# Kernel tuning notes

Hardware: AMD Instinct MI355X
Metric: run time of the kernel (lower is better)

## Reference

```python
import jax, jax.numpy as jnp
import numpy as np

N = 50000        # nodes
E = 800000       # edges (avg degree 16)
IN = 128         # n_feat
C0, H0 = 32, 4   # layer0: out_channels, heads (concat -> 128)
C1, H1 = 32, 1   # layer1: out_channels, heads (mean)
NEG_SLOPE = 0.2


def setup_inputs() -> dict:
    key = jax.random.key(0)
    ks = jax.random.split(key, 16)
    def p(k, shape, fan):
        return jax.random.normal(k, shape, jnp.float32) / np.float32(np.sqrt(fan))
    x = jax.random.normal(ks[0], (N, IN), jnp.float32)
    edge_index = jax.random.randint(ks[1], (2, E), 0, N, dtype=jnp.int32)
    return {
        "x": x,
        "edge_index": edge_index,
        # layer 0 GATConv: in=128 -> 4 heads x 32, concat
        "W0": p(ks[2], (H0 * C0, IN), IN),
        "att_src0": p(ks[3], (H0, C0), C0),
        "att_dst0": p(ks[4], (H0, C0), C0),
        "bias0": jnp.zeros((H0 * C0,), jnp.float32),
        "linW0": p(ks[5], (H0 * C0, IN), IN),
        "linb0": jnp.zeros((H0 * C0,), jnp.float32),
        # layer 1 GATConv: in=128 -> 1 head x 32, mean
        "W1": p(ks[6], (H1 * C1, H0 * C0), H0 * C0),
        "att_src1": p(ks[7], (H1, C1), C1),
        "att_dst1": p(ks[8], (H1, C1), C1),
        "bias1": jnp.zeros((C1,), jnp.float32),
        "linW1": p(ks[9], (C1, H0 * C0), H0 * C0),
        "linb1": jnp.zeros((C1,), jnp.float32),
    }


def gat_conv(x, src, dst, W, att_src, att_dst, bias, concat):
    """PyG-style GATConv (self-loops already appended to src/dst)."""
    n = x.shape[0]
    H, C = att_src.shape
    h = (x @ W.T).reshape(n, H, C)                       # [N,H,C]
    a_src = jnp.einsum('nhc,hc->nh', h, att_src)          # [N,H]
    a_dst = jnp.einsum('nhc,hc->nh', h, att_dst)          # [N,H]
    e = jax.nn.leaky_relu(a_src[src] + a_dst[dst], NEG_SLOPE)  # [E,H]
    # segment softmax over incoming edges of each dst node
    m = jax.ops.segment_max(e, dst, num_segments=n)       # [N,H]
    ex = jnp.exp(e - m[dst])
    denom = jax.ops.segment_sum(ex, dst, num_segments=n)  # [N,H]
    alpha = ex / (denom[dst] + 1e-16)                     # [E,H]
    out = jax.ops.segment_sum(h[src] * alpha[:, :, None], dst, num_segments=n)  # [N,H,C]
    out = out.reshape(n, H * C) if concat else out.mean(axis=1)
    return out + bias


def reference(x, edge_index, W0, att_src0, att_dst0, bias0, linW0, linb0,
              W1, att_src1, att_dst1, bias1, linW1, linb1):
    n = x.shape[0]
    loop = jnp.arange(n, dtype=edge_index.dtype)
    src = jnp.concatenate([edge_index[0], loop])  # add self-loops
    dst = jnp.concatenate([edge_index[1], loop])
    # layer 0: conv + linear skip, then ELU (eval mode -> dropout is a no-op)
    h = gat_conv(x, src, dst, W0, att_src0, att_dst0, bias0, True) + x @ linW0.T + linb0
    h = jax.nn.elu(h)
    # layer 1 (last): conv + linear skip, no activation
    out = gat_conv(h, src, dst, W1, att_src1, att_dst1, bias1, False) + h @ linW1.T + linb1
    return out
```

## Files before the change

kernel.cpp:

```cpp
#include <hip/hip_runtime.h>
#include <hip/hip_bf16.h>


typedef __attribute__((ext_vector_type(8))) short bf8_t;
typedef __attribute__((ext_vector_type(4))) float f4_t;
typedef __attribute__((ext_vector_type(2))) float f2_t;

#define NBUCK 256
#define BCAP  8192
#define TSTR  136

__device__ inline short f2bf(float f) {
    return (short)__builtin_bit_cast(unsigned short, __float2bfloat16(f));
}
__device__ inline float blo(unsigned int p) { return __uint_as_float(p << 16); }
__device__ inline float bhi(unsigned int p) { return __uint_as_float(p & 0xffff0000u); }
__device__ inline float lrexp(float e) {
    e = (e > 0.f) ? e : 0.2f * e;
    return __expf(e);
}

__global__ __launch_bounds__(256) void k_pack(
    const float* __restrict__ W0, const float* __restrict__ lW0,
    const float* __restrict__ W1, const float* __restrict__ lW1,
    const float* __restrict__ b0, const float* __restrict__ lb0,
    const float* __restrict__ b1, const float* __restrict__ lb1,
    short* __restrict__ Wp0, short* __restrict__ lWp0,
    short* __restrict__ Wp1, short* __restrict__ lWp1,
    float* __restrict__ bc0, float* __restrict__ bc1,
    int* __restrict__ gcur) {
    int tid = threadIdx.x;
    int i = blockIdx.x * 256 + tid;
    {
        int j = i & 7, lane = (i >> 3) & 63, kc = i >> 9;
        int kb = kc & 3, ct = kc >> 2;
        int src = (ct * 16 + (lane & 15)) * 128 + kb * 32 + (lane >> 4) * 8 + j;
        Wp0[i]  = f2bf(W0[src]);
        lWp0[i] = f2bf(lW0[src]);
        if (i < 4096) {
            Wp1[i]  = f2bf(W1[src]);
            lWp1[i] = f2bf(lW1[src]);
        }
    }
    if (blockIdx.x == 0) gcur[tid] = 0;
    if (i < 128) bc0[i] = b0[i] + lb0[i];
    else if (i < 160) bc1[i - 128] = b1[i - 128] + lb1[i - 128];
}

__global__ __launch_bounds__(256) void k_bg(
    const int* __restrict__ ei,
    const float* __restrict__ x,
    const short* __restrict__ Wp0, const short* __restrict__ lWp0,
    const float* __restrict__ as0, const float* __restrict__ ad0,
    int* __restrict__ gcur, unsigned int* __restrict__ bucketed,
    unsigned char* __restrict__ h0f8, __hip_bfloat16* __restrict__ skipb,
    float* __restrict__ a0s, float* __restrict__ a0d,
    int E, int T, int NBBK, int N) {
    __shared__ int hist[NBUCK];
    __shared__ int gbase[NBUCK];
    __shared__ short tile[4][16 * TSTR];
    __shared__ unsigned char t8[4][16 * 136];
    int tid = threadIdx.x;

    if ((int)blockIdx.x < NBBK) {
        int bb = blockIdx.x;
        hist[tid] = 0;
        __syncthreads();
        int base = bb * 2048;
        unsigned int pk[8]; int rk[8]; int bk[8];
        #pragma unroll
        for (int j = 0; j < 8; j++) {
            int e = base + j * 256 + tid;
            if (e < T) {
                int src, dst;
                if (e < E) { src = ei[e]; dst = ei[E + e]; }
                else       { src = e - E; dst = src; }
                int b = dst >> 8;
                pk[j] = ((unsigned int)dst << 16) | (unsigned int)src;
                bk[j] = b;
                rk[j] = atomicAdd(&hist[b], 1);
            } else bk[j] = -1;
        }
        __syncthreads();
        int h = hist[tid];
        if (h > 0) gbase[tid] = tid * BCAP + atomicAdd(&gcur[tid], h);
        __syncthreads();
        #pragma unroll
        for (int j = 0; j < 8; j++)
            if (bk[j] >= 0)
                bucketed[gbase[bk[j]] + rk[j]] = pk[j];
        return;
    }

    int bx = blockIdx.x - NBBK;
    int wv = tid >> 6, lane = tid & 63;
    int rowbase = bx * 64 + wv * 16;
    int m = lane & 15, q = lane >> 4;
    int arow = rowbase + m; if (arow >= N) arow = N - 1;
    bf8_t a[4];
    #pragma unroll
    for (int kb = 0; kb < 4; kb++) {
        const float4* px = (const float4*)(x + (size_t)arow * 128 + kb * 32 + q * 8);
        float4 lo = px[0], hi = px[1];
        bf8_t f;
        f[0] = f2bf(lo.x); f[1] = f2bf(lo.y); f[2] = f2bf(lo.z); f[3] = f2bf(lo.w);
        f[4] = f2bf(hi.x); f[5] = f2bf(hi.y); f[6] = f2bf(hi.z); f[7] = f2bf(hi.w);
        a[kb] = f;
    }
    float sacc[4][4], dacc[4][4];
    #pragma unroll
    for (int h = 0; h < 4; h++)
        #pragma unroll
        for (int r = 0; r < 4; r++) { sacc[h][r] = 0.f; dacc[h][r] = 0.f; }
    short* tl = tile[wv];
    unsigned char* t8l = t8[wv];
    int r4 = lane >> 2, qt = lane & 3;
    int drow = rowbase + r4;

    #pragma unroll
    for (int ct = 0; ct < 8; ct++) {
        f4_t acc = {0.f, 0.f, 0.f, 0.f};
        #pragma unroll
        for (int kb = 0; kb < 4; kb++) {
            bf8_t b = *(const bf8_t*)(Wp0 + (((ct * 4 + kb) * 64 + lane) << 3));
            acc = __builtin_amdgcn_mfma_f32_16x16x32_bf16(a[kb], b, acc, 0, 0, 0);
        }
        int hd = ct >> 1;
        float ws = as0[ct * 16 + m], wd = ad0[ct * 16 + m];
        #pragma unroll
        for (int r = 0; r < 4; r++) {
            sacc[hd][r] += acc[r] * ws;
            dacc[hd][r] += acc[r] * wd;
            int pk8 = __builtin_amdgcn_cvt_pk_fp8_f32(acc[r], acc[r], 0, false);
            t8l[(q * 4 + r) * 136 + ct * 16 + m] = (unsigned char)(pk8 & 0xff);
        }
    }
    if (drow < N) {
        const unsigned char* sp8 = t8l + r4 * 136 + qt * 32;
        uint2 w0 = ((const uint2*)sp8)[0];
        uint2 w1 = ((const uint2*)sp8)[1];
        uint2 w2 = ((const uint2*)sp8)[2];
        uint2 w3 = ((const uint2*)sp8)[3];
        uint4 o0 = make_uint4(w0.x, w0.y, w1.x, w1.y);
        uint4 o1 = make_uint4(w2.x, w2.y, w3.x, w3.y);
        unsigned char* dst = h0f8 + (size_t)drow * 128 + qt * 32;
        *(uint4*)dst = o0;
        *(uint4*)(dst + 16) = o1;
    }

    #pragma unroll
    for (int ct = 0; ct < 8; ct++) {
        f4_t acc = {0.f, 0.f, 0.f, 0.f};
        #pragma unroll
        for (int kb = 0; kb < 4; kb++) {
            bf8_t b = *(const bf8_t*)(lWp0 + (((ct * 4 + kb) * 64 + lane) << 3));
            acc = __builtin_amdgcn_mfma_f32_16x16x32_bf16(a[kb], b, acc, 0, 0, 0);
        }
        #pragma unroll
        for (int r = 0; r < 4; r++)
            tl[(q * 4 + r) * TSTR + ct * 16 + m] = f2bf(acc[r]);
    }
    if (drow < N) {
        short* dst = (short*)skipb + (size_t)drow * 128 + qt * 32;
        const short* srcp = tl + r4 * TSTR + qt * 32;
        #pragma unroll
        for (int s = 0; s < 4; s++)
            *(uint4*)(dst + s * 8) = *(const uint4*)(srcp + s * 8);
    }

    #pragma unroll
    for (int h = 0; h < 4; h++)
        #pragma unroll
        for (int r = 0; r < 4; r++) {
            float s = sacc[h][r], d = dacc[h][r];
            #pragma unroll
            for (int off = 1; off < 16; off <<= 1) {
                s += __shfl_xor(s, off);
                d += __shfl_xor(d, off);
            }
            sacc[h][r] = s; dacc[h][r] = d;
        }
    if (m < 4) {
        #pragma unroll
        for (int r = 0; r < 4; r++) {
            int row = rowbase + q * 4 + r;
            if (row < N) {
                float sv = (m == 0) ? sacc[0][r] : (m == 1) ? sacc[1][r]
                         : (m == 2) ? sacc[2][r] : sacc[3][r];
                float dv = (m == 0) ? dacc[0][r] : (m == 1) ? dacc[1][r]
                         : (m == 2) ? dacc[2][r] : dacc[3][r];
                a0s[row * 4 + m] = sv;
                a0d[row * 4 + m] = dv;
            }
        }
    }
}

__global__ __launch_bounds__(256) void k_fill(
    const unsigned int* __restrict__ bucketed, const int* __restrict__ gcur,
    int* __restrict__ rowstart, unsigned short* __restrict__ esrc, int N) {
    __shared__ int ihist[256];
    __shared__ int incl[256];
    int b = blockIdx.x, t = threadIdx.x;
    int nodebase = b << 8;
    int cntt = gcur[t];
    incl[t] = cntt;
    __syncthreads();
    for (int off = 1; off < 256; off <<= 1) {
        int tv = (t >= off) ? incl[t - off] : 0;
        __syncthreads();
        incl[t] += tv;
        __syncthreads();
    }
    int rbase = (b > 0) ? incl[b - 1] : 0;
    if (b == 0 && t == 255) rowstart[N] = incl[255];
    int used = gcur[b];
    const unsigned int* bk = bucketed + (size_t)b * BCAP;
    __syncthreads();
    ihist[t] = 0;
    __syncthreads();
    for (int i = t; i < used; i += 256)
        atomicAdd(&ihist[(bk[i] >> 16) - nodebase], 1);
    __syncthreads();
    int v = ihist[t];
    incl[t] = v;
    __syncthreads();
    for (int off = 1; off < 256; off <<= 1) {
        int tv = (t >= off) ? incl[t - off] : 0;
        __syncthreads();
        incl[t] += tv;
        __syncthreads();
    }
    int myexcl = incl[t] - v;
    int node = nodebase + t;
    if (node < N) rowstart[node] = rbase + myexcl;
    __syncthreads();
    ihist[t] = myexcl;
    __syncthreads();
    for (int i = t; i < used; i += 256) {
        unsigned int p = bk[i];
        int pos = atomicAdd(&ihist[(p >> 16) - nodebase], 1);
        esrc[rbase + pos] = (unsigned short)(p & 0xffffu);
    }
}

__global__ __launch_bounds__(256) void k_aggfuse(
    const int* __restrict__ rowstart, const unsigned short* __restrict__ esrc,
    const uint2* __restrict__ h0f8,
    const float* __restrict__ a0s, const float* __restrict__ a0d,
    const float* __restrict__ bc0,
    const unsigned int* __restrict__ skip0,
    const short* __restrict__ Wp1, const short* __restrict__ lWp1,
    const float* __restrict__ as1, const float* __restrict__ ad1,
    __hip_bfloat16* __restrict__ h1, float* __restrict__ outskip,
    float* __restrict__ a1s, float* __restrict__ a1d, int n) {
    __shared__ __align__(16) short hrow[16][136];
    __shared__ __align__(16) short th[16 * 40];
    __shared__ __align__(16) float ts[16 * 36];
    __shared__ float satt[2][16], datt[2][16];

    int tid = threadIdx.x;
    int nl = tid >> 4, t = tid & 15, hd = t >> 2;
    int rowbase = blockIdx.x << 4;
    int node = rowbase + nl;

    if (node < n) {
        float ad = a0d[node * 4 + hd];
        int s0 = rowstart[node], s1 = rowstart[node + 1];
        float den = 0.f;
        float acc[8];
        #pragma unroll
        for (int k = 0; k < 8; k++) acc[k] = 0.f;
        int i = s0;
        for (; i + 3 < s1; i += 4) {
            int sE[4]; float e[4]; uint2 p[4];
            #pragma unroll
            for (int j = 0; j < 4; j++) sE[j] = esrc[i + j];
            #pragma unroll
            for (int j = 0; j < 4; j++) e[j] = a0s[sE[j] * 4 + hd] + ad;
            #pragma unroll
            for (int j = 0; j < 4; j++) p[j] = h0f8[(size_t)sE[j] * 16 + t];
            #pragma unroll
            for (int j = 0; j < 4; j++) {
                float wgt = lrexp(e[j]);
                den += wgt;
                f2_t c01 = __builtin_amdgcn_cvt_pk_f32_fp8(p[j].x, false);
                f2_t c23 = __builtin_amdgcn_cvt_pk_f32_fp8(p[j].x, true);
                f2_t c45 = __builtin_amdgcn_cvt_pk_f32_fp8(p[j].y, false);
                f2_t c67 = __builtin_amdgcn_cvt_pk_f32_fp8(p[j].y, true);
                acc[0] += wgt * c01.x; acc[1] += wgt * c01.y;
                acc[2] += wgt * c23.x; acc[3] += wgt * c23.y;
                acc[4] += wgt * c45.x; acc[5] += wgt * c45.y;
                acc[6] += wgt * c67.x; acc[7] += wgt * c67.y;
            }
        }
        for (; i < s1; ++i) {
            int s = esrc[i];
            float wgt = lrexp(a0s[s * 4 + hd] + ad);
            uint2 p = h0f8[(size_t)s * 16 + t];
            den += wgt;
            f2_t c01 = __builtin_amdgcn_cvt_pk_f32_fp8(p.x, false);
            f2_t c23 = __builtin_amdgcn_cvt_pk_f32_fp8(p.x, true);
            f2_t c45 = __builtin_amdgcn_cvt_pk_f32_fp8(p.y, false);
            f2_t c67 = __builtin_amdgcn_cvt_pk_f32_fp8(p.y, true);
            acc[0] += wgt * c01.x; acc[1] += wgt * c01.y;
            acc[2] += wgt * c23.x; acc[3] += wgt * c23.y;
            acc[4] += wgt * c45.x; acc[5] += wgt * c45.y;
            acc[6] += wgt * c67.x; acc[7] += wgt * c67.y;
        }
        float inv = 1.0f / (den + 1e-16f);
        uint4 sp = *(const uint4*)(skip0 + (size_t)node * 64 + t * 4);
        int c0 = t * 8;
        float o[8];
        o[0] = acc[0] * inv + blo(sp.x) + bc0[c0 + 0];
        o[1] = acc[1] * inv + bhi(sp.x) + bc0[c0 + 1];
        o[2] = acc[2] * inv + blo(sp.y) + bc0[c0 + 2];
        o[3] = acc[3] * inv + bhi(sp.y) + bc0[c0 + 3];
        o[4] = acc[4] * inv + blo(sp.z) + bc0[c0 + 4];
        o[5] = acc[5] * inv + bhi(sp.z) + bc0[c0 + 5];
        o[6] = acc[6] * inv + blo(sp.w) + bc0[c0 + 6];
        o[7] = acc[7] * inv + bhi(sp.w) + bc0[c0 + 7];
        #pragma unroll
        for (int k = 0; k < 8; k++)
            o[k] = (o[k] > 0.f) ? o[k] : (__expf(o[k]) - 1.f);
        uint4 res;
        res.x = (unsigned int)(unsigned short)f2bf(o[0]) | ((unsigned int)(unsigned short)f2bf(o[1]) << 16);
        res.y = (unsigned int)(unsigned short)f2bf(o[2]) | ((unsigned int)(unsigned short)f2bf(o[3]) << 16);
        res.z = (unsigned int)(unsigned short)f2bf(o[4]) | ((unsigned int)(unsigned short)f2bf(o[5]) << 16);
        res.w = (unsigned int)(unsigned short)f2bf(o[6]) | ((unsigned int)(unsigned short)f2bf(o[7]) << 16);
        *(uint4*)&hrow[nl][t * 8] = res;
    } else {
        *(uint4*)&hrow[nl][t * 8] = make_uint4(0u, 0u, 0u, 0u);
    }
    __syncthreads();

    int wv = tid >> 6, lane = tid & 63;
    int m = lane & 15, q = lane >> 4;
    bf8_t a[4];
    #pragma unroll
    for (int kb = 0; kb < 4; kb++)
        a[kb] = *(const bf8_t*)&hrow[m][kb * 32 + q * 8];
    int ct = wv & 1;
    const short* Wt = (wv < 2) ? Wp1 : lWp1;
    f4_t acc = {0.f, 0.f, 0.f, 0.f};
    #pragma unroll
    for (int kb = 0; kb < 4; kb++) {
        bf8_t b = *(const bf8_t*)(Wt + (((ct * 4 + kb) * 64 + lane) << 3));
        acc = __builtin_amdgcn_mfma_f32_16x16x32_bf16(a[kb], b, acc, 0, 0, 0);
    }
    if (wv < 2) {
        float wsv = as1[ct * 16 + m], wdv = ad1[ct * 16 + m];
        #pragma unroll
        for (int r = 0; r < 4; r++) {
            th[(q * 4 + r) * 40 + ct * 16 + m] = f2bf(acc[r]);
            float s = acc[r] * wsv, d = acc[r] * wdv;
            #pragma unroll
            for (int off = 1; off < 16; off <<= 1) {
                s += __shfl_xor(s, off);
                d += __shfl_xor(d, off);
            }
            if (m == 0) { satt[ct][q * 4 + r] = s; datt[ct][q * 4 + r] = d; }
        }
    } else {
        #pragma unroll
        for (int r = 0; r < 4; r++)
            ts[(q * 4 + r) * 36 + ct * 16 + m] = acc[r];
    }
    __syncthreads();

    if (tid < 64) {
        int row = tid >> 2, qt = tid & 3;
        if (rowbase + row < n)
            *(uint4*)((short*)h1 + (size_t)(rowbase + row) * 32 + qt * 8) =
                *(const uint4*)&th[row * 40 + qt * 8];
    } else if (tid < 192) {
        int i2 = tid - 64, row = i2 >> 3, qt = i2 & 7;
        if (rowbase + row < n)
            *(uint4*)(outskip + (size_t)(rowbase + row) * 32 + qt * 4) =
                *(const uint4*)&ts[row * 36 + qt * 4];
    } else if (tid < 208) {
        int r2 = tid - 192;
        if (rowbase + r2 < n) {
            a1s[rowbase + r2] = satt[0][r2] + satt[1][r2];
            a1d[rowbase + r2] = datt[0][r2] + datt[1][r2];
        }
    }
}

__global__ __launch_bounds__(256) void k_agg1(
    const int* __restrict__ rowstart, const unsigned short* __restrict__ esrc,
    const __hip_bfloat16* __restrict__ h1,
    const float* __restrict__ a1s, const float* __restrict__ a1d,
    const float* __restrict__ bc1,
    float* __restrict__ out, int n) {
    int node = (blockIdx.x * 256 + threadIdx.x) >> 6;
    int lane = threadIdx.x & 63;
    if (node >= n) return;
    int g = lane >> 4, t = lane & 15;
    float ad = a1d[node];
    int s0 = rowstart[node], s1 = rowstart[node + 1];
    const unsigned int* h1w = (const unsigned int*)h1;
    float den = 0.f, acc0 = 0.f, acc1 = 0.f;
    int i = s0 + g;
    for (; i + 12 < s1; i += 16) {
        int sE[4]; float e[4]; unsigned int p[4];
        #pragma unroll
        for (int j = 0; j < 4; j++) sE[j] = esrc[i + 4 * j];
        #pragma unroll
        for (int j = 0; j < 4; j++) e[j] = a1s[sE[j]] + ad;
        #pragma unroll
        for (int j = 0; j < 4; j++) p[j] = h1w[(size_t)sE[j] * 16 + t];
        #pragma unroll
        for (int j = 0; j < 4; j++) {
            float wgt = lrexp(e[j]);
            den += wgt;
            acc0 += wgt * blo(p[j]);
            acc1 += wgt * bhi(p[j]);
        }
    }
    for (; i < s1; i += 4) {
        int s = esrc[i];
        float wv = lrexp(a1s[s] + ad);
        unsigned int p = h1w[(size_t)s * 16 + t];
        den += wv; acc0 += wv * blo(p); acc1 += wv * bhi(p);
    }
    acc0 += __shfl_xor(acc0, 16); acc0 += __shfl_xor(acc0, 32);
    acc1 += __shfl_xor(acc1, 16); acc1 += __shfl_xor(acc1, 32);
    den  += __shfl_xor(den, 16);  den  += __shfl_xor(den, 32);
    if (g == 0) {
        float inv = 1.0f / (den + 1e-16f);
        int c0 = t * 2;
        size_t idx = (size_t)node * 32 + c0;
        float2 sk = *(const float2*)(out + idx);
        float2 r;
        r.x = acc0 * inv + sk.x + bc1[c0];
        r.y = acc1 * inv + sk.y + bc1[c0 + 1];
        *(float2*)(out + idx) = r;
    }
}


extern "C" void kernel_launch(void* const* d_in, const int* in_sizes, int n_in,
                              void* d_out, int out_size, void* d_ws, size_t ws_size,
                              hipStream_t stream) {
    const float* x   = (const float*)d_in[0];
    const int*   ei  = (const int*)d_in[1];
    const float* W0  = (const float*)d_in[2];
    const float* as0 = (const float*)d_in[3];
    const float* ad0 = (const float*)d_in[4];
    const float* b0  = (const float*)d_in[5];
    const float* lW0 = (const float*)d_in[6];
    const float* lb0 = (const float*)d_in[7];
    const float* W1  = (const float*)d_in[8];
    const float* as1 = (const float*)d_in[9];
    const float* ad1 = (const float*)d_in[10];
    const float* b1  = (const float*)d_in[11];
    const float* lW1 = (const float*)d_in[12];
    const float* lb1 = (const float*)d_in[13];
    float* out = (float*)d_out;

    const int N = in_sizes[0] / 128;
    const int E = in_sizes[1] / 2;
    const int T = E + N;
    const int NBK  = (N + 255) >> 8;
    const int NBBK = (T + 2047) / 2048;
    const int NG0  = (N + 63) / 64;

    char* w = (char*)d_ws;
    auto alloc = [&](size_t bytes) -> char* {
        char* p = w; w += (bytes + 255) / 256 * 256; return p;
    };
    int* rowstart  = (int*)alloc((size_t)(N + 1) * 4);
    int* gcur      = (int*)alloc(NBUCK * 4);
    unsigned int* bucketed = (unsigned int*)alloc((size_t)NBUCK * BCAP * 4);
    unsigned short* esrc = (unsigned short*)alloc((size_t)T * 2);
    float* aS      = (float*)alloc((size_t)N * 4 * 4);
    float* aD      = (float*)alloc((size_t)N * 4 * 4);
    char* hbuf     = alloc((size_t)N * 128);
    __hip_bfloat16* skip0 = (__hip_bfloat16*)alloc((size_t)N * 128 * 2);
    __hip_bfloat16* h1buf = (__hip_bfloat16*)alloc((size_t)N * 32 * 2);
    float* aS1     = (float*)alloc((size_t)N * 4);
    float* aD1     = (float*)alloc((size_t)N * 4);
    short* Wp0  = (short*)alloc(16384 * 2);
    short* lWp0 = (short*)alloc(16384 * 2);
    short* Wp1  = (short*)alloc(4096 * 2);
    short* lWp1 = (short*)alloc(4096 * 2);
    float* bc0  = (float*)alloc(128 * 4);
    float* bc1  = (float*)alloc(32 * 4);

    k_pack<<<64, 256, 0, stream>>>(W0, lW0, W1, lW1, b0, lb0, b1, lb1,
                                   Wp0, lWp0, Wp1, lWp1, bc0, bc1, gcur);
    k_bg<<<NBBK + NG0, 256, 0, stream>>>(
        ei, x, Wp0, lWp0, as0, ad0, gcur, bucketed,
        (unsigned char*)hbuf, skip0, aS, aD, E, T, NBBK, N);
    k_fill<<<NBK, 256, 0, stream>>>(bucketed, gcur, rowstart, esrc, N);
    k_aggfuse<<<(N + 15) / 16, 256, 0, stream>>>(
        rowstart, esrc, (const uint2*)hbuf, aS, aD, bc0,
        (const unsigned int*)skip0, Wp1, lWp1, as1, ad1,
        h1buf, out, aS1, aD1, N);
    k_agg1<<<(N + 3) / 4, 256, 0, stream>>>(rowstart, esrc, h1buf,
                                            aS1, aD1, bc1, out, N);
}
```

Measured before the change: 198.0 us.

## Split layer-0 GEMM across bucketing and fill kernels to overlap stages

Moves the layer-0 GEMM body into a shared device function and splits its rows. The first GSPLIT rows still run in the bucketing kernel, and the rest run as extra blocks in the CSR fill kernel. This lets the small, sync-heavy fill kernel (196 blocks) share the GPU with GEMM work so the machine stays busier. LDS is merged into one aliased buffer, which needs an added __syncthreads between the fp8 and bf16 tile phases. The hardcoded split point assumes N is above GSPLIT and tunes the load balance to this input size.

```diff
diff --git a/kernel.cpp b/kernel.cpp
--- a/kernel.cpp
+++ b/kernel.cpp
@@ -9,6 +9,7 @@
 #define NBUCK 256
 #define BCAP  8192
 #define TSTR  136
+#define GSPLIT 29952
 
 __device__ inline short f2bf(float f) {
     return (short)__builtin_bit_cast(unsigned short, __float2bfloat16(f));
@@ -47,6 +48,118 @@
     else if (i < 160) bc1[i - 128] = b1[i - 128] + lb1[i - 128];
 }
 
+__device__ __forceinline__ void gemm0_block(
+    int rowbase0, int tid, char* lds,
+    const float* __restrict__ x,
+    const short* __restrict__ Wp0, const short* __restrict__ lWp0,
+    const float* __restrict__ as0, const float* __restrict__ ad0,
+    unsigned char* __restrict__ h0f8, __hip_bfloat16* __restrict__ skipb,
+    float* __restrict__ a0s, float* __restrict__ a0d, int N) {
+    int wv = tid >> 6, lane = tid & 63;
+    int rowbase = rowbase0 + wv * 16;
+    int m = lane & 15, q = lane >> 4;
+    int arow = rowbase + m; if (arow >= N) arow = N - 1;
+    bf8_t a[4];
+    #pragma unroll
+    for (int kb = 0; kb < 4; kb++) {
+        const float4* px = (const float4*)(x + (size_t)arow * 128 + kb * 32 + q * 8);
+        float4 lo = px[0], hi = px[1];
+        bf8_t f;
+        f[0] = f2bf(lo.x); f[1] = f2bf(lo.y); f[2] = f2bf(lo.z); f[3] = f2bf(lo.w);
+        f[4] = f2bf(hi.x); f[5] = f2bf(hi.y); f[6] = f2bf(hi.z); f[7] = f2bf(hi.w);
+        a[kb] = f;
+    }
+    float sacc[4][4], dacc[4][4];
+    #pragma unroll
+    for (int h = 0; h < 4; h++)
+        #pragma unroll
+        for (int r = 0; r < 4; r++) { sacc[h][r] = 0.f; dacc[h][r] = 0.f; }
+    char* wslice = lds + wv * 4352;
+    short* tl = (short*)wslice;
+    unsigned char* t8l = (unsigned char*)wslice;
+    int r4 = lane >> 2, qt = lane & 3;
+    int drow = rowbase + r4;
+
+    #pragma unroll
+    for (int ct = 0; ct < 8; ct++) {
+        f4_t acc = {0.f, 0.f, 0.f, 0.f};
+        #pragma unroll
+        for (int kb = 0; kb < 4; kb++) {
+            bf8_t b = *(const bf8_t*)(Wp0 + (((ct * 4 + kb) * 64 + lane) << 3));
+            acc = __builtin_amdgcn_mfma_f32_16x16x32_bf16(a[kb], b, acc, 0, 0, 0);
+        }
+        int hd = ct >> 1;
+        float ws = as0[ct * 16 + m], wd = ad0[ct * 16 + m];
+        #pragma unroll
+        for (int r = 0; r < 4; r++) {
+            sacc[hd][r] += acc[r] * ws;
+            dacc[hd][r] += acc[r] * wd;
+            int pk8 = __builtin_amdgcn_cvt_pk_fp8_f32(acc[r], acc[r], 0, false);
+            t8l[(q * 4 + r) * 136 + ct * 16 + m] = (unsigned char)(pk8 & 0xff);
+        }
+    }
+    if (drow < N) {
+        const unsigned char* sp8 = t8l + r4 * 136 + qt * 32;
+        uint2 w0 = ((const uint2*)sp8)[0];
+        uint2 w1 = ((const uint2*)sp8)[1];
+        uint2 w2 = ((const uint2*)sp8)[2];
+        uint2 w3 = ((const uint2*)sp8)[3];
+        uint4 o0 = make_uint4(w0.x, w0.y, w1.x, w1.y);
+        uint4 o1 = make_uint4(w2.x, w2.y, w3.x, w3.y);
+        unsigned char* dst = h0f8 + (size_t)drow * 128 + qt * 32;
+        *(uint4*)dst = o0;
+        *(uint4*)(dst + 16) = o1;
+    }
+    __syncthreads();
+
+    #pragma unroll
+    for (int ct = 0; ct < 8; ct++) {
+        f4_t acc = {0.f, 0.f, 0.f, 0.f};
+        #pragma unroll
+        for (int kb = 0; kb < 4; kb++) {
+            bf8_t b = *(const bf8_t*)(lWp0 + (((ct * 4 + kb) * 64 + lane) << 3));
+            acc = __builtin_amdgcn_mfma_f32_16x16x32_bf16(a[kb], b, acc, 0, 0, 0);
+        }
+        #pragma unroll
+        for (int r = 0; r < 4; r++)
+            tl[(q * 4 + r) * TSTR + ct * 16 + m] = f2bf(acc[r]);
+    }
+    if (drow < N) {
+        short* dst = (short*)skipb + (size_t)drow * 128 + qt * 32;
+        const short* srcp = tl + r4 * TSTR + qt * 32;
+        #pragma unroll
+        for (int s = 0; s < 4; s++)
+            *(uint4*)(dst + s * 8) = *(const uint4*)(srcp + s * 8);
+    }
+
+    #pragma unroll
+    for (int h = 0; h < 4; h++)
+        #pragma unroll
+        for (int r = 0; r < 4; r++) {
+            float s = sacc[h][r], d = dacc[h][r];
+            #pragma unroll
+            for (int off = 1; off < 16; off <<= 1) {
+                s += __shfl_xor(s, off);
+                d += __shfl_xor(d, off);
+            }
+            sacc[h][r] = s; dacc[h][r] = d;
+        }
+    if (m < 4) {
+        #pragma unroll
+        for (int r = 0; r < 4; r++) {
+            int row = rowbase + q * 4 + r;
+            if (row < N) {
+                float sv = (m == 0) ? sacc[0][r] : (m == 1) ? sacc[1][r]
+                         : (m == 2) ? sacc[2][r] : sacc[3][r];
+                float dv = (m == 0) ? dacc[0][r] : (m == 1) ? dacc[1][r]
+                         : (m == 2) ? dacc[2][r] : dacc[3][r];
+                a0s[row * 4 + m] = sv;
+                a0d[row * 4 + m] = dv;
+            }
+        }
+    }
+}
+
 __global__ __launch_bounds__(256) void k_bg(
     const int* __restrict__ ei,
     const float* __restrict__ x,
@@ -56,13 +169,12 @@
     unsigned char* __restrict__ h0f8, __hip_bfloat16* __restrict__ skipb,
     float* __restrict__ a0s, float* __restrict__ a0d,
     int E, int T, int NBBK, int N) {
-    __shared__ int hist[NBUCK];
-    __shared__ int gbase[NBUCK];
-    __shared__ short tile[4][16 * TSTR];
-    __shared__ unsigned char t8[4][16 * 136];
+    __shared__ __align__(16) char lds[17408];
     int tid = threadIdx.x;
 
     if ((int)blockIdx.x < NBBK) {
+        int* hist  = (int*)lds;
+        int* gbase = (int*)(lds + 1024);
         int bb = blockIdx.x;
         hist[tid] = 0;
         __syncthreads();
@@ -92,156 +204,73 @@
         return;
     }
 
-    int bx = blockIdx.x - NBBK;
-    int wv = tid >> 6, lane = tid & 63;
-    int rowbase = bx * 64 + wv * 16;
-    int m = lane & 15, q = lane >> 4;
-    int arow = rowbase + m; if (arow >= N) arow = N - 1;
-    bf8_t a[4];
-    #pragma unroll
-    for (int kb = 0; kb < 4; kb++) {
-        const float4* px = (const float4*)(x + (size_t)arow * 128 + kb * 32 + q * 8);
-        float4 lo = px[0], hi = px[1];
-        bf8_t f;
-        f[0] = f2bf(lo.x); f[1] = f2bf(lo.y); f[2] = f2bf(lo.z); f[3] = f2bf(lo.w);
-        f[4] = f2bf(hi.x); f[5] = f2bf(hi.y); f[6] = f2bf(hi.z); f[7] = f2bf(hi.w);
-        a[kb] = f;
-    }
-    float sacc[4][4], dacc[4][4];
-    #pragma unroll
-    for (int h = 0; h < 4; h++)
-        #pragma unroll
-        for (int r = 0; r < 4; r++) { sacc[h][r] = 0.f; dacc[h][r] = 0.f; }
-    short* tl = tile[wv];
-    unsigned char* t8l = t8[wv];
-    int r4 = lane >> 2, qt = lane & 3;
-    int drow = rowbase + r4;
-
-    #pragma unroll
-    for (int ct = 0; ct < 8; ct++) {
-        f4_t acc = {0.f, 0.f, 0.f, 0.f};
-        #pragma unroll
-        for (int kb = 0; kb < 4; kb++) {
-            bf8_t b = *(const bf8_t*)(Wp0 + (((ct * 4 + kb) * 64 + lane) << 3));
-            acc = __builtin_amdgcn_mfma_f32_16x16x32_bf16(a[kb], b, acc, 0, 0, 0);
-        }
-        int hd = ct >> 1;
-        float ws = as0[ct * 16 + m], wd = ad0[ct * 16 + m];
-        #pragma unroll
-        for (int r = 0; r < 4; r++) {
-            sacc[hd][r] += acc[r] * ws;
-            dacc[hd][r] += acc[r] * wd;
-            int pk8 = __builtin_amdgcn_cvt_pk_fp8_f32(acc[r], acc[r], 0, false);
-            t8l[(q * 4 + r) * 136 + ct * 16 + m] = (unsigned char)(pk8 & 0xff);
-        }
-    }
-    if (drow < N) {
-        const unsigned char* sp8 = t8l + r4 * 136 + qt * 32;
-        uint2 w0 = ((const uint2*)sp8)[0];
-        uint2 w1 = ((const uint2*)sp8)[1];
-        uint2 w2 = ((const uint2*)sp8)[2];
-        uint2 w3 = ((const uint2*)sp8)[3];
-        uint4 o0 = make_uint4(w0.x, w0.y, w1.x, w1.y);
-        uint4 o1 = make_uint4(w2.x, w2.y, w3.x, w3.y);
-        unsigned char* dst = h0f8 + (size_t)drow * 128 + qt * 32;
-        *(uint4*)dst = o0;
-        *(uint4*)(dst + 16) = o1;
-    }
-
-    #pragma unroll
-    for (int ct = 0; ct < 8; ct++) {
-        f4_t acc = {0.f, 0.f, 0.f, 0.f};
-        #pragma unroll
-        for (int kb = 0; kb < 4; kb++) {
-            bf8_t b = *(const bf8_t*)(lWp0 + (((ct * 4 + kb) * 64 + lane) << 3));
-            acc = __builtin_amdgcn_mfma_f32_16x16x32_bf16(a[kb], b, acc, 0, 0, 0);
-        }
-        #pragma unroll
-        for (int r = 0; r < 4; r++)
-            tl[(q * 4 + r) * TSTR + ct * 16 + m] = f2bf(acc[r]);
-    }
-    if (drow < N) {
-        short* dst = (short*)skipb + (size_t)drow * 128 + qt * 32;
-        const short* srcp = tl + r4 * TSTR + qt * 32;
-        #pragma unroll
-        for (int s = 0; s < 4; s++)
-            *(uint4*)(dst + s * 8) = *(const uint4*)(srcp + s * 8);
-    }
-
-    #pragma unroll
-    for (int h = 0; h < 4; h++)
-        #pragma unroll
-        for (int r = 0; r < 4; r++) {
-            float s = sacc[h][r], d = dacc[h][r];
-            #pragma unroll
-            for (int off = 1; off < 16; off <<= 1) {
-                s += __shfl_xor(s, off);
-                d += __shfl_xor(d, off);
-            }
-            sacc[h][r] = s; dacc[h][r] = d;
-        }
-    if (m < 4) {
-        #pragma unroll
-        for (int r = 0; r < 4; r++) {
-            int row = rowbase + q * 4 + r;
-            if (row < N) {
-                float sv = (m == 0) ? sacc[0][r] : (m == 1) ? sacc[1][r]
-                         : (m == 2) ? sacc[2][r] : sacc[3][r];
-                float dv = (m == 0) ? dacc[0][r] : (m == 1) ? dacc[1][r]
-                         : (m == 2) ? dacc[2][r] : dacc[3][r];
-                a0s[row * 4 + m] = sv;
-                a0d[row * 4 + m] = dv;
-            }
-        }
-    }
-}
-
-__global__ __launch_bounds__(256) void k_fill(
+    int rowbase0 = (blockIdx.x - NBBK) * 64;
+    gemm0_block(rowbase0, tid, lds, x, Wp0, lWp0, as0, ad0,
+                h0f8, skipb, a0s, a0d, N);
+}
+
+__global__ __launch_bounds__(256) void k_fg(
     const unsigned int* __restrict__ bucketed, const int* __restrict__ gcur,
-    int* __restrict__ rowstart, unsigned short* __restrict__ esrc, int N) {
-    __shared__ int ihist[256];
-    __shared__ int incl[256];
-    int b = blockIdx.x, t = threadIdx.x;
-    int nodebase = b << 8;
-    int cntt = gcur[t];
-    incl[t] = cntt;
-    __syncthreads();
-    for (int off = 1; off < 256; off <<= 1) {
-        int tv = (t >= off) ? incl[t - off] : 0;
-        __syncthreads();
-        incl[t] += tv;
-        __syncthreads();
-    }
-    int rbase = (b > 0) ? incl[b - 1] : 0;
-    if (b == 0 && t == 255) rowstart[N] = incl[255];
-    int used = gcur[b];
-    const unsigned int* bk = bucketed + (size_t)b * BCAP;
-    __syncthreads();
-    ihist[t] = 0;
-    __syncthreads();
-    for (int i = t; i < used; i += 256)
-        atomicAdd(&ihist[(bk[i] >> 16) - nodebase], 1);
-    __syncthreads();
-    int v = ihist[t];
-    incl[t] = v;
-    __syncthreads();
-    for (int off = 1; off < 256; off <<= 1) {
-        int tv = (t >= off) ? incl[t - off] : 0;
-        __syncthreads();
-        incl[t] += tv;
-        __syncthreads();
-    }
-    int myexcl = incl[t] - v;
-    int node = nodebase + t;
-    if (node < N) rowstart[node] = rbase + myexcl;
-    __syncthreads();
-    ihist[t] = myexcl;
-    __syncthreads();
-    for (int i = t; i < used; i += 256) {
-        unsigned int p = bk[i];
-        int pos = atomicAdd(&ihist[(p >> 16) - nodebase], 1);
-        esrc[rbase + pos] = (unsigned short)(p & 0xffffu);
-    }
+    int* __restrict__ rowstart, unsigned short* __restrict__ esrc,
+    const float* __restrict__ x,
+    const short* __restrict__ Wp0, const short* __restrict__ lWp0,
+    const float* __restrict__ as0, const float* __restrict__ ad0,
+    unsigned char* __restrict__ h0f8, __hip_bfloat16* __restrict__ skipb,
+    float* __restrict__ a0s, float* __restrict__ a0d,
+    int NBK, int N) {
+    __shared__ __align__(16) char lds[17408];
+    int tid = threadIdx.x;
+
+    if ((int)blockIdx.x < NBK) {
+        int* ihist = (int*)lds;
+        int* incl  = (int*)(lds + 1024);
+        int b = blockIdx.x, t = tid;
+        int nodebase = b << 8;
+        int cntt = gcur[t];
+        incl[t] = cntt;
+        __syncthreads();
+        for (int off = 1; off < 256; off <<= 1) {
+            int tv = (t >= off) ? incl[t - off] : 0;
+            __syncthreads();
+            incl[t] += tv;
+            __syncthreads();
+        }
+        int rbase = (b > 0) ? incl[b - 1] : 0;
+        if (b == 0 && t == 255) rowstart[N] = incl[255];
+        int used = gcur[b];
+        const unsigned int* bk = bucketed + (size_t)b * BCAP;
+        __syncthreads();
+        ihist[t] = 0;
+        __syncthreads();
+        for (int i = t; i < used; i += 256)
+            atomicAdd(&ihist[(bk[i] >> 16) - nodebase], 1);
+        __syncthreads();
+        int v = ihist[t];
+        incl[t] = v;
+        __syncthreads();
+        for (int off = 1; off < 256; off <<= 1) {
+            int tv = (t >= off) ? incl[t - off] : 0;
+            __syncthreads();
+            incl[t] += tv;
+            __syncthreads();
+        }
+        int myexcl = incl[t] - v;
+        int node = nodebase + t;
+        if (node < N) rowstart[node] = rbase + myexcl;
+        __syncthreads();
+        ihist[t] = myexcl;
+        __syncthreads();
+        for (int i = t; i < used; i += 256) {
+            unsigned int p = bk[i];
+            int pos = atomicAdd(&ihist[(p >> 16) - nodebase], 1);
+            esrc[rbase + pos] = (unsigned short)(p & 0xffffu);
+        }
+        return;
+    }
+
+    int rowbase0 = GSPLIT + (blockIdx.x - NBK) * 64;
+    gemm0_block(rowbase0, tid, lds, x, Wp0, lWp0, as0, ad0,
+                h0f8, skipb, a0s, a0d, N);
 }
 
 __global__ __launch_bounds__(256) void k_aggfuse(
@@ -464,7 +493,8 @@
     const int T = E + N;
     const int NBK  = (N + 255) >> 8;
     const int NBBK = (T + 2047) / 2048;
-    const int NG0  = (N + 63) / 64;
+    const int NG0A = GSPLIT / 64;
+    const int NG0B = (N - GSPLIT + 63) / 64;
 
     char* w = (char*)d_ws;
     auto alloc = [&](size_t bytes) -> char* {
@@ -490,10 +520,13 @@
 
     k_pack<<<64, 256, 0, stream>>>(W0, lW0, W1, lW1, b0, lb0, b1, lb1,
                                    Wp0, lWp0, Wp1, lWp1, bc0, bc1, gcur);
-    k_bg<<<NBBK + NG0, 256, 0, stream>>>(
+    k_bg<<<NBBK + NG0A, 256, 0, stream>>>(
         ei, x, Wp0, lWp0, as0, ad0, gcur, bucketed,
         (unsigned char*)hbuf, skip0, aS, aD, E, T, NBBK, N);
-    k_fill<<<NBK, 256, 0, stream>>>(bucketed, gcur, rowstart, esrc, N);
+    k_fg<<<NBK + NG0B, 256, 0, stream>>>(
+        bucketed, gcur, rowstart, esrc,
+        x, Wp0, lWp0, as0, ad0,
+        (unsigned char*)hbuf, skip0, aS, aD, NBK, N);
     k_aggfuse<<<(N + 15) / 16, 256, 0, stream>>>(
         rowstart, esrc, (const uint2*)hbuf, aS, aD, bc0,
         (const unsigned int*)skip0, Wp1, lWp1, as1, ad1,
```

New measurement: 195.5 us. No clear change (-1.3%).
